# Kernel tuning notes

Hardware: AMD Instinct MI355X
Metric: run time of the kernel (lower is better)

Reference implementation:

```python
import jax, jax.numpy as jnp
import numpy as np
import math

N = 512
H = 512
L = 16384
R_MIN, R_MAX, MAX_PHASE = 0.0, 1.0, 6.283


def setup_inputs() -> dict:
    key = jax.random.key(0)
    ks = jax.random.split(key, 8)
    u1 = jax.random.uniform(ks[0], (N,))
    u2 = jax.random.uniform(ks[1], (N,))
    nu_log = jnp.log(-0.5 * jnp.log(u1 * (R_MAX ** 2 - R_MIN ** 2) + R_MIN ** 2))
    theta_log = jnp.log(u2 * MAX_PHASE)
    B_re = jax.random.normal(ks[2], (N, H)) / math.sqrt(2 * H)
    B_im = jax.random.normal(ks[3], (N, H)) / math.sqrt(2 * H)
    C_re = jax.random.normal(ks[4], (H, N)) / math.sqrt(N)
    C_im = jax.random.normal(ks[5], (H, N)) / math.sqrt(N)
    D = jax.random.normal(ks[6], (H,))
    diag_lambda = jnp.exp(-jnp.exp(nu_log) + 1j * jnp.exp(theta_log))
    gamma_log = jnp.log(jnp.sqrt(1.0 - jnp.abs(diag_lambda) ** 2))
    x = jax.random.normal(ks[7], (L, H), dtype=jnp.float32)
    # state is Lambda's multiplier in the original code; ones => standard LRU
    state_re = jnp.ones((N,), dtype=jnp.float32)
    state_im = jnp.zeros((N,), dtype=jnp.float32)
    return {"x": x, "state_re": state_re, "state_im": state_im,
            "nu_log": nu_log, "theta_log": theta_log, "gamma_log": gamma_log,
            "B_re": B_re, "B_im": B_im, "C_re": C_re, "C_im": C_im, "D": D}


def _binop(ei, ej):
    a_i, bu_i = ei
    a_j, bu_j = ej
    return (a_j * a_i, a_j * bu_i + bu_j)


def reference(x, state_re, state_im, nu_log, theta_log, gamma_log,
              B_re, B_im, C_re, C_im, D):
    Lambda = jnp.exp(-jnp.exp(nu_log) + 1j * jnp.exp(theta_log))  # (N,) c64
    # NOTE: original uses exp(i*gamma_log) (a phase), faithful here
    exp_gamma = jnp.exp(1j * gamma_log.astype(jnp.complex64))      # (N,)
    B = (B_re + 1j * B_im) * exp_gamma[:, None]                    # (N,H)
    C = C_re + 1j * C_im                                           # (H,N)
    state = state_re + 1j * state_im                               # (N,)
    a0 = Lambda * state                                            # (N,)
    a_elems = jnp.broadcast_to(a0, (x.shape[0], a0.shape[0]))      # (L,N)
    xc = x.astype(jnp.complex64)                                   # (L,H)
    Bu = xc @ B.T                                                  # (L,N)
    _, inner_states = jax.lax.associative_scan(_binop, (a_elems, Bu))
    y = jnp.real(inner_states @ C.T) + D[None, :] * x              # (L,H)
    return y
```

## Files before the change

kernel.cpp:

```cpp
#include <hip/hip_runtime.h>
#include <hip/hip_bf16.h>
#include <cstdint>

#define L_SEQ 16384
#define NST   512
#define HDIM  512
#define CH    512
#define CT    32

typedef __attribute__((ext_vector_type(8))) short short8;
typedef __attribute__((ext_vector_type(4))) float f32x4;

static __device__ __forceinline__ ushort f2bf(float f) {
  union { float f; unsigned int u; } v; v.f = f;
  unsigned int r = v.u + 0x7fffu + ((v.u >> 16) & 1u);
  return (ushort)(r >> 16);
}
static __device__ __forceinline__ float bf2f(ushort u) {
  union { unsigned int u; float f; } v; v.u = ((unsigned int)u) << 16;
  return v.f;
}

static __device__ __forceinline__ void mfma_16x16x32_bf16(f32x4& d, short8 a, short8 b) {
  asm("v_mfma_f32_16x16x32_bf16 %0, %1, %2, %0" : "+v"(d) : "v"(a), "v"(b));
}

static __device__ __forceinline__ void gload_lds16(const ushort* g, ushort* l) {
  __builtin_amdgcn_global_load_lds((__attribute__((address_space(1))) void*)(g),
                                   (__attribute__((address_space(3))) void*)(l),
                                   16, 0, 0);
}

__global__ __launch_bounds__(256) void setup_all(
    const float* __restrict__ st_re, const float* __restrict__ st_im,
    const float* __restrict__ nu_log, const float* __restrict__ theta_log,
    const float* __restrict__ gamma_log,
    const float* __restrict__ B_re, const float* __restrict__ B_im,
    const float* __restrict__ C_re, const float* __restrict__ C_im,
    const float* __restrict__ X,
    float2* __restrict__ lam, float2* __restrict__ lamT,
    ushort* __restrict__ W1, ushort* __restrict__ W2,
    ushort* __restrict__ xb)
{
  int bid = blockIdx.x, tid = threadIdx.x;
  if (bid < 4096) {
    size_t i = ((size_t)bid * 256 + tid) * 8;
#pragma unroll
    for (int j = 0; j < 8; j += 4) {
      float4 v = *(const float4*)(X + i + j);
      ushort4 o;
      o.x = f2bf(v.x); o.y = f2bf(v.y); o.z = f2bf(v.z); o.w = f2bf(v.w);
      *(ushort4*)(xb + i + j) = o;
    }
  } else if (bid < 5120) {
    int idx = (bid - 4096) * 256 + tid;
    int n = idx >> 9, h = idx & 511;
    float g = gamma_log[n];
    float sg, cg; sincosf(g, &sg, &cg);
    float br = B_re[idx], bi = B_im[idx];
    W1[(size_t)n * 512 + h]         = f2bf(br * cg - bi * sg);
    W1[(size_t)(n + 512) * 512 + h] = f2bf(br * sg + bi * cg);
  } else if (bid < 6144) {
    int idx = (bid - 5120) * 256 + tid;
    int hh = idx >> 9, n = idx & 511;
    W2[(size_t)hh * 1024 + n]       = f2bf(C_re[idx]);
    W2[(size_t)hh * 1024 + 512 + n] = f2bf(-C_im[idx]);
  } else {
    int n = (bid - 6144) * 256 + tid;
    float nu  = expf(nu_log[n]);
    float th  = expf(theta_log[n]);
    float mag = expf(-nu);
    float sth, cth; sincosf(th, &sth, &cth);
    float lr = mag * cth, li = mag * sth;
    float sr = st_re[n], si = st_im[n];
    float ar = lr * sr - li * si;
    float ai = lr * si + li * sr;
    lam[n] = make_float2(ar, ai);
    float pr = ar, pi = ai;
#pragma unroll
    for (int i = 0; i < 5; ++i) {
      float nr = pr * pr - pi * pi;
      float ni = 2.f * pr * pi;
      pr = nr; pi = ni;
    }
    lamT[n] = make_float2(pr, pi);
  }
}

template <int BM, int BN, int WMW, int WNW, int EPI>
__global__ __launch_bounds__(WMW * WNW * 64, 2)
void gemm_p(const ushort* __restrict__ A, const ushort* __restrict__ Bm,
            ushort* __restrict__ Cb, float* __restrict__ Cf,
            const float* __restrict__ Dv, const float* __restrict__ X,
            int M, int Ncols, int K)
{
  constexpr int THREADS = WMW * WNW * 64;
  constexpr int FM = BM / (WMW * 16);
  constexpr int FN = BN / (WNW * 16);
  constexpr int SLOT = (BM + BN) * 32;
  constexpr int GR = (BM + BN) * 4;
  constexpr int LPT = GR / THREADS;
  static_assert(LPT == 4, "vmcnt immediates assume 4 loads/thread/tile");
  __shared__ __align__(16) ushort lds[4 * SLOT];

  const int t = threadIdx.x, lane = t & 63, w = t >> 6;
  const int wr = w / WNW, wc = w % WNW;
  const int m0 = blockIdx.x * BM, n0 = blockIdx.y * BN;
  const int rr = lane & 15, kk = (lane >> 4) * 8;
  const int swzu = ((rr >> 1) & 3) << 3;
  const int NK = K / 32;

  f32x4 acc[FM][FN];
#pragma unroll
  for (int i = 0; i < FM; ++i)
#pragma unroll
    for (int j = 0; j < FN; ++j) { f32x4 z = {0.f, 0.f, 0.f, 0.f}; acc[i][j] = z; }

  auto stage = [&](int kt) {
    int k0 = kt * 32;
    ushort* base = lds + (kt & 3) * SLOT;
#pragma unroll
    for (int j = 0; j < LPT; ++j) {
      int d = j * THREADS + t;
      const ushort* g;
      if (d < BM * 4) {
        int row = d >> 2;
        int sl  = (d & 3) ^ ((row >> 1) & 3);
        g = A + (size_t)(m0 + row) * K + k0 + sl * 8;
      } else {
        int dd = d - BM * 4;
        int row = dd >> 2;
        int sl  = (dd & 3) ^ ((row >> 1) & 3);
        g = Bm + (size_t)(n0 + row) * K + k0 + sl * 8;
      }
      gload_lds16(g, base + d * 8);
    }
  };

  stage(0); stage(1); stage(2);
  asm volatile("s_waitcnt vmcnt(8)" ::: "memory");
  asm volatile("s_barrier" ::: "memory");

  for (int kt = 0; kt < NK; ++kt) {
    const ushort* As = lds + (kt & 3) * SLOT;
    const ushort* Bs = As + BM * 32;
    short8 af[FM], bb[FN];
#pragma unroll
    for (int mi = 0; mi < FM; ++mi)
      af[mi] = *(const short8*)(As + (wr * FM * 16 + mi * 16 + rr) * 32 + (kk ^ swzu));
#pragma unroll
    for (int ni = 0; ni < FN; ++ni)
      bb[ni] = *(const short8*)(Bs + (wc * FN * 16 + ni * 16 + rr) * 32 + (kk ^ swzu));
    if (kt + 3 < NK) stage(kt + 3);
    asm volatile("s_waitcnt lgkmcnt(0)" ::: "memory");
    __builtin_amdgcn_sched_barrier(0);
    __builtin_amdgcn_s_setprio(1);
#pragma unroll
    for (int mi = 0; mi < FM; ++mi)
#pragma unroll
      for (int ni = 0; ni < FN; ++ni)
        mfma_16x16x32_bf16(acc[mi][ni], af[mi], bb[ni]);
    __builtin_amdgcn_s_setprio(0);
    __builtin_amdgcn_sched_barrier(0);
    if (kt < NK - 3)       asm volatile("s_waitcnt vmcnt(8)" ::: "memory");
    else if (kt == NK - 3) asm volatile("s_waitcnt vmcnt(4)" ::: "memory");
    else                   asm volatile("s_waitcnt vmcnt(0)" ::: "memory");
    asm volatile("s_barrier" ::: "memory");
  }

  const int crow = (lane >> 4) * 4, ccol = lane & 15;
#pragma unroll
  for (int mi = 0; mi < FM; ++mi) {
#pragma unroll
    for (int ni = 0; ni < FN; ++ni) {
      int col = n0 + wc * FN * 16 + ni * 16 + ccol;
#pragma unroll
      for (int r = 0; r < 4; ++r) {
        int row = m0 + wr * FM * 16 + mi * 16 + crow + r;
        float v = acc[mi][ni][r];
        size_t idx = (size_t)row * Ncols + col;
        if (EPI == 0) Cb[idx] = f2bf(v);
        else          Cf[idx] = v + Dv[col] * X[idx];
      }
    }
  }
}

__global__ __launch_bounds__(256) void scanA(const ushort* __restrict__ Bu,
                                             const float2* __restrict__ lam,
                                             float2* __restrict__ carry)
{
  int q = threadIdx.x;
  int c = blockIdx.x;
  float2 a0 = lam[2 * q], a1 = lam[2 * q + 1];
  float cr0 = 0.f, ci0 = 0.f, cr1 = 0.f, ci1 = 0.f;
  const ushort* base = Bu + (size_t)c * CT * 1024 + 2 * q;
#pragma unroll 4
  for (int tt = 0; tt < CT; ++tt) {
    ushort2 re = *(const ushort2*)(base + tt * 1024);
    ushort2 im = *(const ushort2*)(base + tt * 1024 + 512);
    float br0 = bf2f(re.x), br1 = bf2f(re.y);
    float bi0 = bf2f(im.x), bi1 = bf2f(im.y);
    float nr0 = a0.x * cr0 - a0.y * ci0 + br0;
    float ni0 = a0.x * ci0 + a0.y * cr0 + bi0;
    cr0 = nr0; ci0 = ni0;
    float nr1 = a1.x * cr1 - a1.y * ci1 + br1;
    float ni1 = a1.x * ci1 + a1.y * cr1 + bi1;
    cr1 = nr1; ci1 = ni1;
  }
  carry[(size_t)(2 * q) * CH + c]     = make_float2(cr0, ci0);
  carry[(size_t)(2 * q + 1) * CH + c] = make_float2(cr1, ci1);
}

__global__ __launch_bounds__(CH) void scanC(const float2* __restrict__ carry,
                                            const float2* __restrict__ lamT,
                                            float2* __restrict__ prefix)
{
  int n = blockIdx.x;
  int c = threadIdx.x;
  __shared__ float2 buf[CH];
  float2 aT = lamT[n];
  float2 v = carry[(size_t)n * CH + c];
  buf[c] = v;
  __syncthreads();
  float mr = aT.x, mi = aT.y;
#pragma unroll
  for (int s = 1; s < CH; s <<= 1) {
    float2 o = make_float2(0.f, 0.f);
    if (c >= s) o = buf[c - s];
    __syncthreads();
    v.x += mr * o.x - mi * o.y;
    v.y += mr * o.y + mi * o.x;
    buf[c] = v;
    __syncthreads();
    float nmr = mr * mr - mi * mi;
    float nmi = 2.f * mr * mi;
    mr = nmr; mi = nmi;
  }
  float2 p = (c == 0) ? make_float2(0.f, 0.f) : buf[c - 1];
  prefix[(size_t)n * CH + c] = p;
}

__global__ __launch_bounds__(256) void scanB(ushort* __restrict__ Bu,
                                             const float2* __restrict__ lam,
                                             const float2* __restrict__ prefix)
{
  int q = threadIdx.x;
  int c = blockIdx.x;
  float2 a0 = lam[2 * q], a1 = lam[2 * q + 1];
  float2 g0 = prefix[(size_t)(2 * q) * CH + c];
  float2 g1 = prefix[(size_t)(2 * q + 1) * CH + c];
  float hr0 = g0.x, hi0 = g0.y, hr1 = g1.x, hi1 = g1.y;
  ushort* base = Bu + (size_t)c * CT * 1024 + 2 * q;
#pragma unroll 4
  for (int tt = 0; tt < CT; ++tt) {
    ushort2 re = *(const ushort2*)(base + tt * 1024);
    ushort2 im = *(const ushort2*)(base + tt * 1024 + 512);
    float nr0 = a0.x * hr0 - a0.y * hi0 + bf2f(re.x);
    float ni0 = a0.x * hi0 + a0.y * hr0 + bf2f(im.x);
    hr0 = nr0; hi0 = ni0;
    float nr1 = a1.x * hr1 - a1.y * hi1 + bf2f(re.y);
    float ni1 = a1.x * hi1 + a1.y * hr1 + bf2f(im.y);
    hr1 = nr1; hi1 = ni1;
    ushort2 ore, oim;
    ore.x = f2bf(hr0); ore.y = f2bf(hr1);
    oim.x = f2bf(hi0); oim.y = f2bf(hi1);
    *(ushort2*)(base + tt * 1024)       = ore;
    *(ushort2*)(base + tt * 1024 + 512) = oim;
  }
}

extern "C" void kernel_launch(void* const* d_in, const int* in_sizes, int n_in,
                              void* d_out, int out_size, void* d_ws, size_t ws_size,
                              hipStream_t stream)
{
  const float* x         = (const float*)d_in[0];
  const float* state_re  = (const float*)d_in[1];
  const float* state_im  = (const float*)d_in[2];
  const float* nu_log    = (const float*)d_in[3];
  const float* theta_log = (const float*)d_in[4];
  const float* gamma_log = (const float*)d_in[5];
  const float* B_re      = (const float*)d_in[6];
  const float* B_im      = (const float*)d_in[7];
  const float* C_re      = (const float*)d_in[8];
  const float* C_im      = (const float*)d_in[9];
  const float* Dv        = (const float*)d_in[10];
  float* y = (float*)d_out;

  char* ws = (char*)d_ws;
  size_t off = 0;
  float2* lam    = (float2*)(ws + off); off += 4096;
  float2* lamT   = (float2*)(ws + off); off += 4096;
  float2* carry  = (float2*)(ws + off); off += (size_t)CH * NST * sizeof(float2);
  float2* prefix = (float2*)(ws + off); off += (size_t)CH * NST * sizeof(float2);
  ushort* W1 = (ushort*)(ws + off); off += (size_t)2 * NST * HDIM * sizeof(ushort);
  ushort* W2 = (ushort*)(ws + off); off += (size_t)HDIM * 2 * NST * sizeof(ushort);
  ushort* xb = (ushort*)(ws + off); off += (size_t)L_SEQ * HDIM * sizeof(ushort);
  ushort* Bu = (ushort*)(ws + off); off += (size_t)L_SEQ * 2 * NST * sizeof(ushort);

  setup_all<<<6146, 256, 0, stream>>>(state_re, state_im, nu_log, theta_log,
                                      gamma_log, B_re, B_im, C_re, C_im, x,
                                      lam, lamT, W1, W2, xb);

  gemm_p<256, 256, 2, 4, 0><<<dim3(L_SEQ / 256, (2 * NST) / 256), 512, 0, stream>>>(
      xb, W1, Bu, nullptr, nullptr, nullptr, L_SEQ, 2 * NST, HDIM);

  scanA<<<CH, 256, 0, stream>>>(Bu, lam, carry);
  scanC<<<NST, CH, 0, stream>>>(carry, lamT, prefix);
  scanB<<<CH, 256, 0, stream>>>(Bu, lam, prefix);

  gemm_p<128, 128, 2, 2, 1><<<dim3(L_SEQ / 128, HDIM / 128), 256, 0, stream>>>(
      Bu, W2, nullptr, y, Dv, x, L_SEQ, HDIM, 2 * NST);
}
```

Before: 89.92 us.

## Fuse chunk-carry scan into first GEMM epilogue and interleave complex layout

The standalone scanA kernel is removed. Its per-chunk carry recurrence now runs in the epilogue of the first GEMM, which reads back its own freshly written Bu tile after a barrier, while that tile is likely still in cache. The W1 and W2 layouts change so the real and imaginary parts of each state sit next to each other, which lets scanB use single ushort4 loads and stores. The final epilogue reads the bf16 copy of x instead of fp32 x to halve that read traffic, at the cost of some precision in the D*x term.

```diff
diff --git a/kernel.cpp b/kernel.cpp
--- a/kernel.cpp
+++ b/kernel.cpp
@@ -30,6 +30,7 @@
                                    (__attribute__((address_space(3))) void*)(l),
                                    16, 0, 0);
 }
+
 
 __global__ __launch_bounds__(256) void setup_all(
     const float* __restrict__ st_re, const float* __restrict__ st_im,
@@ -58,13 +59,13 @@
     float g = gamma_log[n];
     float sg, cg; sincosf(g, &sg, &cg);
     float br = B_re[idx], bi = B_im[idx];
-    W1[(size_t)n * 512 + h]         = f2bf(br * cg - bi * sg);
-    W1[(size_t)(n + 512) * 512 + h] = f2bf(br * sg + bi * cg);
+    W1[(size_t)(2 * n) * 512 + h]     = f2bf(br * cg - bi * sg);
+    W1[(size_t)(2 * n + 1) * 512 + h] = f2bf(br * sg + bi * cg);
   } else if (bid < 6144) {
     int idx = (bid - 5120) * 256 + tid;
     int hh = idx >> 9, n = idx & 511;
-    W2[(size_t)hh * 1024 + n]       = f2bf(C_re[idx]);
-    W2[(size_t)hh * 1024 + 512 + n] = f2bf(-C_im[idx]);
+    W2[(size_t)hh * 1024 + 2 * n]     = f2bf(C_re[idx]);
+    W2[(size_t)hh * 1024 + 2 * n + 1] = f2bf(-C_im[idx]);
   } else {
     int n = (bid - 6144) * 256 + tid;
     float nu  = expf(nu_log[n]);
@@ -91,7 +92,8 @@
 __global__ __launch_bounds__(WMW * WNW * 64, 2)
 void gemm_p(const ushort* __restrict__ A, const ushort* __restrict__ Bm,
             ushort* __restrict__ Cb, float* __restrict__ Cf,
-            const float* __restrict__ Dv, const float* __restrict__ X,
+            const float* __restrict__ Dv, const ushort* __restrict__ Xb,
+            const float2* __restrict__ lam, float2* __restrict__ carry,
             int M, int Ncols, int K)
 {
   constexpr int THREADS = WMW * WNW * 64;
@@ -180,36 +182,32 @@
         float v = acc[mi][ni][r];
         size_t idx = (size_t)row * Ncols + col;
         if (EPI == 0) Cb[idx] = f2bf(v);
-        else          Cf[idx] = v + Dv[col] * X[idx];
+        else          Cf[idx] = v + Dv[col] * bf2f(Xb[idx]);
       }
     }
   }
-}
-
-__global__ __launch_bounds__(256) void scanA(const ushort* __restrict__ Bu,
-                                             const float2* __restrict__ lam,
-                                             float2* __restrict__ carry)
-{
-  int q = threadIdx.x;
-  int c = blockIdx.x;
-  float2 a0 = lam[2 * q], a1 = lam[2 * q + 1];
-  float cr0 = 0.f, ci0 = 0.f, cr1 = 0.f, ci1 = 0.f;
-  const ushort* base = Bu + (size_t)c * CT * 1024 + 2 * q;
-#pragma unroll 4
-  for (int tt = 0; tt < CT; ++tt) {
-    ushort2 re = *(const ushort2*)(base + tt * 1024);
-    ushort2 im = *(const ushort2*)(base + tt * 1024 + 512);
-    float br0 = bf2f(re.x), br1 = bf2f(re.y);
-    float bi0 = bf2f(im.x), bi1 = bf2f(im.y);
-    float nr0 = a0.x * cr0 - a0.y * ci0 + br0;
-    float ni0 = a0.x * ci0 + a0.y * cr0 + bi0;
-    cr0 = nr0; ci0 = ni0;
-    float nr1 = a1.x * cr1 - a1.y * ci1 + br1;
-    float ni1 = a1.x * ci1 + a1.y * cr1 + bi1;
-    cr1 = nr1; ci1 = ni1;
-  }
-  carry[(size_t)(2 * q) * CH + c]     = make_float2(cr0, ci0);
-  carry[(size_t)(2 * q + 1) * CH + c] = make_float2(cr1, ci1);
+
+  if (EPI == 0) {
+    asm volatile("s_waitcnt vmcnt(0)" ::: "memory");
+    __syncthreads();
+#pragma unroll
+    for (int task = 0; task < 2; ++task) {
+      int c  = (t >> 7) + task * 4;
+      int ch = t & 127;
+      float2 a = lam[(n0 >> 1) + ch];
+      float cr = 0.f, ci = 0.f;
+      const ushort* p = Cb + (size_t)(m0 + c * 32) * Ncols + n0 + 2 * ch;
+#pragma unroll 8
+      for (int r = 0; r < 32; ++r) {
+        ushort2 v = *(const ushort2*)(p + (size_t)r * Ncols);
+        float br = bf2f(v.x), bi = bf2f(v.y);
+        float nr = a.x * cr - a.y * ci + br;
+        float ni = a.x * ci + a.y * cr + bi;
+        cr = nr; ci = ni;
+      }
+      carry[(size_t)((n0 >> 1) + ch) * CH + (m0 >> 5) + c] = make_float2(cr, ci);
+    }
+  }
 }
 
 __global__ __launch_bounds__(CH) void scanC(const float2* __restrict__ carry,
@@ -251,22 +249,20 @@
   float2 g0 = prefix[(size_t)(2 * q) * CH + c];
   float2 g1 = prefix[(size_t)(2 * q + 1) * CH + c];
   float hr0 = g0.x, hi0 = g0.y, hr1 = g1.x, hi1 = g1.y;
-  ushort* base = Bu + (size_t)c * CT * 1024 + 2 * q;
+  ushort* base = Bu + (size_t)c * CT * 1024 + 4 * q;
 #pragma unroll 4
   for (int tt = 0; tt < CT; ++tt) {
-    ushort2 re = *(const ushort2*)(base + tt * 1024);
-    ushort2 im = *(const ushort2*)(base + tt * 1024 + 512);
-    float nr0 = a0.x * hr0 - a0.y * hi0 + bf2f(re.x);
-    float ni0 = a0.x * hi0 + a0.y * hr0 + bf2f(im.x);
+    ushort4 v = *(const ushort4*)(base + tt * 1024);
+    float nr0 = a0.x * hr0 - a0.y * hi0 + bf2f(v.x);
+    float ni0 = a0.x * hi0 + a0.y * hr0 + bf2f(v.y);
     hr0 = nr0; hi0 = ni0;
-    float nr1 = a1.x * hr1 - a1.y * hi1 + bf2f(re.y);
-    float ni1 = a1.x * hi1 + a1.y * hr1 + bf2f(im.y);
+    float nr1 = a1.x * hr1 - a1.y * hi1 + bf2f(v.z);
+    float ni1 = a1.x * hi1 + a1.y * hr1 + bf2f(v.w);
     hr1 = nr1; hi1 = ni1;
-    ushort2 ore, oim;
-    ore.x = f2bf(hr0); ore.y = f2bf(hr1);
-    oim.x = f2bf(hi0); oim.y = f2bf(hi1);
-    *(ushort2*)(base + tt * 1024)       = ore;
-    *(ushort2*)(base + tt * 1024 + 512) = oim;
+    ushort4 o;
+    o.x = f2bf(hr0); o.y = f2bf(hi0);
+    o.z = f2bf(hr1); o.w = f2bf(hi1);
+    *(ushort4*)(base + tt * 1024) = o;
   }
 }
 
@@ -303,12 +299,11 @@
                                       lam, lamT, W1, W2, xb);
 
   gemm_p<256, 256, 2, 4, 0><<<dim3(L_SEQ / 256, (2 * NST) / 256), 512, 0, stream>>>(
-      xb, W1, Bu, nullptr, nullptr, nullptr, L_SEQ, 2 * NST, HDIM);
-
-  scanA<<<CH, 256, 0, stream>>>(Bu, lam, carry);
+      xb, W1, Bu, nullptr, nullptr, nullptr, lam, carry, L_SEQ, 2 * NST, HDIM);
+
   scanC<<<NST, CH, 0, stream>>>(carry, lamT, prefix);
   scanB<<<CH, 256, 0, stream>>>(Bu, lam, prefix);
 
   gemm_p<128, 128, 2, 2, 1><<<dim3(L_SEQ / 128, HDIM / 128), 256, 0, stream>>>(
-      Bu, W2, nullptr, y, Dv, x, L_SEQ, HDIM, 2 * NST);
-}
+      Bu, W2, nullptr, y, Dv, xb, nullptr, nullptr, L_SEQ, HDIM, 2 * NST);
+}
```

New measurement: 84.99 us. 1.06x faster.
